# Kernel optimization log

Measured on AMD Instinct MI355X. Metric: run time of the kernel, lower is better.

## Reference

```python
import jax, jax.numpy as jnp
import numpy as np

N_NODES = 100000
N_EDGES = 1600000
IN_DIM = 128
HID = 64
OUT_DIM = 3


def _glorot(key, shape):
    fan_in, fan_out = shape[0], shape[1]
    std = (2.0 / (fan_in + fan_out)) ** 0.5
    return jax.random.normal(key, shape, jnp.float32) * std


def setup_inputs() -> dict:
    key = jax.random.key(0)
    ks = jax.random.split(key, 12)
    x = jax.random.normal(ks[0], (N_NODES, IN_DIM), jnp.float32)
    edge_index = jax.random.randint(ks[1], (2, N_EDGES), 0, N_NODES, dtype=jnp.int32)
    return {
        "x": x,
        "edge_index": edge_index,
        "W1": _glorot(ks[2], (IN_DIM, HID)), "b1": jnp.zeros((HID,), jnp.float32),
        "W2": _glorot(ks[3], (HID, HID)), "b2": jnp.zeros((HID,), jnp.float32),
        "W3": _glorot(ks[4], (HID, HID)), "b3": jnp.zeros((HID,), jnp.float32),
        "W4": _glorot(ks[5], (HID, HID // 2)), "b4": jnp.zeros((HID // 2,), jnp.float32),
        "Wh": _glorot(ks[6], (HID // 2, OUT_DIM)), "bh": jnp.zeros((OUT_DIM,), jnp.float32),
    }


def reference(x, edge_index, W1, b1, W2, b2, W3, b3, W4, b4, Wh, bh):
    n = x.shape[0]
    self_loops = jnp.arange(n, dtype=edge_index.dtype)
    src = jnp.concatenate([edge_index[0], self_loops])  # message sources j
    dst = jnp.concatenate([edge_index[1], self_loops])  # aggregation targets i
    # symmetric GCN normalization with self-loops: deg over targets (unit edge weights)
    deg = jax.ops.segment_sum(jnp.ones_like(dst, jnp.float32), dst, num_segments=n)
    dinv = jnp.where(deg > 0, jax.lax.rsqrt(deg), 0.0)
    norm = dinv[src] * dinv[dst]  # [E+N]

    def gcn(h, W, b):
        h = h @ W  # transform first (PyG GCNConv order)
        agg = jax.ops.segment_sum(h[src] * norm[:, None], dst, num_segments=n)
        return agg + b

    h = jax.nn.relu(gcn(x, W1, b1))   # dropout is identity in eval mode
    h = jax.nn.relu(gcn(h, W2, b2))
    h = jax.nn.relu(gcn(h, W3, b3))
    h = jax.nn.relu(gcn(h, W4, b4))
    return h @ Wh + bh  # [N, 3]
```

## Files before the change

kernel.cpp:

```cpp
#include <hip/hip_runtime.h>
#include <hip/hip_bf16.h>
#include <hip/hip_fp16.h>
#include <cstdint>


#define MAXD 512
#define EB   8192
#define PADSLACK 2048

typedef _Float16 half8v __attribute__((ext_vector_type(8)));
typedef _Float16 half2v __attribute__((ext_vector_type(2)));
typedef float    float4v __attribute__((ext_vector_type(4)));

#if defined(__has_builtin)
#if __has_builtin(__builtin_amdgcn_fdot2)
#define HAVE_FDOT2 1
#endif
#endif

__device__ __forceinline__ float fdot2f(half2v a, half2v b, float c) {
#ifdef HAVE_FDOT2
    return __builtin_amdgcn_fdot2(a, b, c, false);
#else
    return c + (float)a[0] * (float)b[0] + (float)a[1] * (float)b[1];
#endif
}

__device__ __forceinline__ void digit_base_scan(const int* __restrict__ totals,
                                                int ND, int* pairs, int* cbs) {
    const int t = threadIdx.x;
    const int e0 = 2 * t, e1 = 2 * t + 1;
    int v0 = (e0 < ND) ? totals[e0] : 0;
    int v1 = (e1 < ND) ? totals[e1] : 0;
    pairs[t] = v0 + v1;
    __syncthreads();
    for (int off = 1; off < 256; off <<= 1) {
        int x = (t >= off) ? pairs[t - off] : 0;
        __syncthreads();
        pairs[t] += x;
        __syncthreads();
    }
    int ep = pairs[t] - v0 - v1;
    cbs[e0] = ep;
    cbs[e1] = ep + v0;
    __syncthreads();
}

__device__ __forceinline__ void hist_body(const int* __restrict__ ei,
                                          int* __restrict__ histM, int E, int b) {
    __shared__ int hist[MAXD];
    const int tid = threadIdx.x;
    hist[tid] = 0; hist[tid + 256] = 0;
    __syncthreads();
    const int base = b * EB;
#pragma unroll 2
    for (int it = 0; it < EB / 256; it += 4) {
        int d[4]; bool ok[4];
#pragma unroll
        for (int u = 0; u < 4; ++u) {
            int e = base + (it + u) * 256 + tid;
            ok[u] = e < E;
            d[u] = ok[u] ? ei[E + e] : 0;
        }
#pragma unroll
        for (int u = 0; u < 4; ++u)
            if (ok[u]) atomicAdd(&hist[d[u] >> 8], 1);
    }
    __syncthreads();
    histM[(size_t)b * MAXD + tid] = hist[tid];
    histM[(size_t)b * MAXD + tid + 256] = hist[tid + 256];
}

__global__ __launch_bounds__(256) void scan_digits_k(int* __restrict__ histM,
                                                     int* __restrict__ totals,
                                                     int NBLK) {
    __shared__ int s[256];
    const int t = threadIdx.x, dg = blockIdx.x;
    int v = (t < NBLK) ? histM[(size_t)t * MAXD + dg] : 0;
    s[t] = v;
    __syncthreads();
    for (int off = 1; off < 256; off <<= 1) {
        int x = (t >= off) ? s[t - off] : 0;
        __syncthreads();
        s[t] += x;
        __syncthreads();
    }
    if (t < NBLK) histM[(size_t)t * MAXD + dg] = s[t] - v;
    if (t == 255) totals[dg] = s[255];
}

template <int K, int OUT>
__device__ __forceinline__ void gemm_body(const float* __restrict__ H,
                                          const float* __restrict__ W,
                                          float* __restrict__ Tout, int n, int bx) {
    constexpr int TX  = OUT / 4;
    constexpr int TY  = 256 / TX;
    constexpr int BM  = TY * 4;
    constexpr int BK  = 32;
    constexpr int PAD = 4;

    __shared__ float At[BK][BM + PAD];
    __shared__ float Ws[BK][OUT];

    const int t    = threadIdx.x;
    const int cx   = t % TX;
    const int ry   = t / TX;
    const int row0 = bx * BM;

    float acc[4][4] = {{0.f}};
    const int arow = t >> 3;
    const int af4  = t & 7;

    for (int k0 = 0; k0 < K; k0 += BK) {
#pragma unroll
        for (int p = 0; p < BM / 32; ++p) {
            int r  = arow + p * 32;
            int gr = row0 + r;
            int grc = gr < n ? gr : n - 1;
            float4 v = *reinterpret_cast<const float4*>(
                H + (size_t)grc * K + k0 + af4 * 4);
            At[af4 * 4 + 0][r] = v.x;
            At[af4 * 4 + 1][r] = v.y;
            At[af4 * 4 + 2][r] = v.z;
            At[af4 * 4 + 3][r] = v.w;
        }
#pragma unroll
        for (int p = 0; p < (BK * OUT) / 1024; ++p) {
            int idx = t + p * 256;
            int wk  = idx / (OUT / 4);
            int wf  = idx % (OUT / 4);
            float4 v = *reinterpret_cast<const float4*>(
                W + (size_t)(k0 + wk) * OUT + wf * 4);
            *reinterpret_cast<float4*>(&Ws[wk][wf * 4]) = v;
        }
        __syncthreads();
#pragma unroll
        for (int k = 0; k < BK; ++k) {
            float4 a = *reinterpret_cast<const float4*>(&At[k][ry * 4]);
            float4 w = *reinterpret_cast<const float4*>(&Ws[k][cx * 4]);
            acc[0][0] = fmaf(a.x, w.x, acc[0][0]);
            acc[0][1] = fmaf(a.x, w.y, acc[0][1]);
            acc[0][2] = fmaf(a.x, w.z, acc[0][2]);
            acc[0][3] = fmaf(a.x, w.w, acc[0][3]);
            acc[1][0] = fmaf(a.y, w.x, acc[1][0]);
            acc[1][1] = fmaf(a.y, w.y, acc[1][1]);
            acc[1][2] = fmaf(a.y, w.z, acc[1][2]);
            acc[1][3] = fmaf(a.y, w.w, acc[1][3]);
            acc[2][0] = fmaf(a.z, w.x, acc[2][0]);
            acc[2][1] = fmaf(a.z, w.y, acc[2][1]);
            acc[2][2] = fmaf(a.z, w.z, acc[2][2]);
            acc[2][3] = fmaf(a.z, w.w, acc[2][3]);
            acc[3][0] = fmaf(a.w, w.x, acc[3][0]);
            acc[3][1] = fmaf(a.w, w.y, acc[3][1]);
            acc[3][2] = fmaf(a.w, w.z, acc[3][2]);
            acc[3][3] = fmaf(a.w, w.w, acc[3][3]);
        }
        __syncthreads();
    }
#pragma unroll
    for (int i = 0; i < 4; ++i) {
        int gr = row0 + ry * 4 + i;
        if (gr < n) {
            float4 v = make_float4(acc[i][0], acc[i][1], acc[i][2], acc[i][3]);
            *reinterpret_cast<float4*>(Tout + (size_t)gr * OUT + cx * 4) = v;
        }
    }
}

__device__ __forceinline__ void pack_body(const int* __restrict__ ei,
                                          const int* __restrict__ histM,
                                          const int* __restrict__ totals,
                                          int* __restrict__ packed,
                                          int E, int ND, int b) {
    __shared__ int pairs[256];
    __shared__ int cbs[MAXD];
    __shared__ int cur[MAXD];
    const int tid = threadIdx.x;
    digit_base_scan(totals, ND, pairs, cbs);
    for (int t = tid; t < ND; t += 256)
        cur[t] = cbs[t] + histM[(size_t)b * MAXD + t];
    __syncthreads();
    const int base = b * EB;
    for (int it = 0; it < EB / 256; it += 4) {
        int s[4], d[4]; bool ok[4];
#pragma unroll
        for (int u = 0; u < 4; ++u) {
            int e = base + (it + u) * 256 + tid;
            ok[u] = e < E;
            if (ok[u]) { s[u] = ei[e]; d[u] = ei[E + e]; }
        }
#pragma unroll
        for (int u = 0; u < 4; ++u) {
            if (ok[u]) {
                int pos = atomicAdd(&cur[d[u] >> 8], 1);
                packed[pos] = (s[u] << 8) | (d[u] & 255);
            }
        }
    }
}

__global__ __launch_bounds__(256) void hist_gemm1_k(
    const int* __restrict__ ei, int* __restrict__ histM, int E,
    const float* __restrict__ x, const float* __restrict__ W1,
    float* __restrict__ T1, int n, int NH) {
    const int bx = blockIdx.x;
    if (bx < NH) hist_body(ei, histM, E, bx);
    else         gemm_body<128, 64>(x, W1, T1, n, bx - NH);
}

__global__ __launch_bounds__(256) void pack_gemm1_k(
    const int* __restrict__ ei, const int* __restrict__ histM,
    const int* __restrict__ totals, int* __restrict__ packed,
    const float* __restrict__ x, const float* __restrict__ W1,
    float* __restrict__ T1, int n, int E, int ND, int NPB, int G1) {
    const int bx = blockIdx.x;
    if (bx < NPB) pack_body(ei, histM, totals, packed, E, ND, bx);
    else          gemm_body<128, 64>(x, W1, T1, n, G1 + bx - NPB);
}

__global__ __launch_bounds__(256) void bucket_k(const int* __restrict__ packed,
                                                const int* __restrict__ totals,
                                                int ND,
                                                int* __restrict__ col,
                                                int* __restrict__ rowptr,
                                                int* __restrict__ counts,
                                                float* __restrict__ dinv,
                                                const float* __restrict__ Traw,
                                                __half* __restrict__ Th, int n) {
    __shared__ int   pairs[256];
    __shared__ int   cbs[MAXD];
    __shared__ int   hist[256];
    __shared__ int   pref[256];
    __shared__ int   cur[256];
    __shared__ float dinv_l[256];

    const int tid = threadIdx.x;
    const int dg  = blockIdx.x;
    digit_base_scan(totals, ND, pairs, cbs);
    const int base  = cbs[dg];
    const int m     = totals[dg];
    const int basep = base + dg * PADSLACK;

    hist[tid] = 0;
    __syncthreads();
    for (int k0 = 0; k0 < m; k0 += 1024) {
        int v[4]; bool ok[4];
#pragma unroll
        for (int u = 0; u < 4; ++u) {
            int k = k0 + u * 256 + tid;
            ok[u] = k < m;
            v[u] = ok[u] ? packed[base + k] : 0;
        }
#pragma unroll
        for (int u = 0; u < 4; ++u)
            if (ok[u]) atomicAdd(&hist[v[u] & 255], 1);
    }
    __syncthreads();
    const int deg   = hist[tid];
    const int cnt_p = (deg + 8) & ~7;
    pref[tid] = cnt_p;
    __syncthreads();
    for (int off = 1; off < 256; off <<= 1) {
        int x = (tid >= off) ? pref[tid - off] : 0;
        __syncthreads();
        pref[tid] += x;
        __syncthreads();
    }
    const int rp = basep + pref[tid] - cnt_p;
    const float di = rsqrtf((float)(deg + 1));
    dinv_l[tid] = di;
    cur[tid] = rp + 1;
    const int d = dg * 256 + tid;
    if (d < n) {
        counts[d] = cnt_p;
        dinv[d]   = di;
        rowptr[d] = rp;
        col[rp]   = d;
        for (int k = deg + 1; k < cnt_p; ++k) col[rp + k] = n;
    }
    __syncthreads();
    for (int k0 = 0; k0 < m; k0 += 1024) {
        int v[4]; bool ok[4];
#pragma unroll
        for (int u = 0; u < 4; ++u) {
            int k = k0 + u * 256 + tid;
            ok[u] = k < m;
            v[u] = ok[u] ? packed[base + k] : 0;
        }
#pragma unroll
        for (int u = 0; u < 4; ++u) {
            if (ok[u]) {
                int pos = atomicAdd(&cur[v[u] & 255], 1);
                col[pos] = v[u] >> 8;
            }
        }
    }
    const int r0 = dg * 256;
#pragma unroll 4
    for (int it = 0; it < 16; ++it) {
        int idx = it * 256 + tid;
        int rl  = idx >> 4;
        int r   = r0 + rl;
        if (r < n) {
            float4 v = reinterpret_cast<const float4*>(Traw)[(size_t)r * 16 + (idx & 15)];
            float dd = dinv_l[rl];
            union { ushort4 u; __half h[4]; } pk;
            pk.h[0] = __float2half_rn(v.x * dd);
            pk.h[1] = __float2half_rn(v.y * dd);
            pk.h[2] = __float2half_rn(v.z * dd);
            pk.h[3] = __float2half_rn(v.w * dd);
            reinterpret_cast<ushort4*>(Th)[(size_t)r * 16 + (idx & 15)] = pk.u;
        }
    }
    if (dg == 0 && tid < 16) {
        uint2 z; z.x = 0u; z.y = 0u;
        reinterpret_cast<uint2*>(Th)[(size_t)n * 16 + tid] = z;
    }
}

template <int OUT>
__global__ __launch_bounds__(256) void gemm_mfma_k(
    const _Float16* __restrict__ H, const float* __restrict__ W,
    const float* __restrict__ dinv, _Float16* __restrict__ T, int n) {
    constexpr int NT = OUT / 16;
    const int lane = threadIdx.x & 63;
    const int m16  = lane & 15;
    const int quad = lane >> 4;
    const int wid  = (blockIdx.x * blockDim.x + threadIdx.x) >> 6;
    const int nw   = (gridDim.x * blockDim.x) >> 6;

    half8v bfrag[NT][2];
#pragma unroll
    for (int t = 0; t < NT; ++t)
#pragma unroll
        for (int h = 0; h < 2; ++h)
#pragma unroll
            for (int j = 0; j < 8; ++j)
                bfrag[t][h][j] = (_Float16)W[(size_t)(h * 32 + quad * 8 + j) * OUT
                                             + t * 16 + m16];

    const int nblk = (n + 15) >> 4;
    for (int rb = wid; rb < nblk; rb += nw) {
        const int r0 = rb * 16;
        int ra = r0 + m16; if (ra >= n) ra = n - 1;
        const half8v* hrow = reinterpret_cast<const half8v*>(H + (size_t)ra * 64);
        half8v a0 = hrow[quad];
        half8v a1 = hrow[4 + quad];

        float4v dfr[NT];
#pragma unroll
        for (int t = 0; t < NT; ++t) {
            float4v z = {0.f, 0.f, 0.f, 0.f};
            z = __builtin_amdgcn_mfma_f32_16x16x32_f16(a0, bfrag[t][0], z, 0, 0, 0);
            z = __builtin_amdgcn_mfma_f32_16x16x32_f16(a1, bfrag[t][1], z, 0, 0, 0);
            dfr[t] = z;
        }
#pragma unroll
        for (int reg = 0; reg < 4; ++reg) {
            int row = r0 + quad * 4 + reg;
            if (row < n) {
                float di = dinv[row];
#pragma unroll
                for (int t = 0; t < NT; ++t)
                    T[(size_t)row * 64 + t * 16 + m16] =
                        (_Float16)(dfr[t][reg] * di);
            }
        }
    }
}

template <int NB, int LR>
__device__ __forceinline__ void gather_batch(int c_l, const uint2* __restrict__ T2,
                                             int q, int sw, float4& acc) {
    constexpr int NSW = 64 / LR;
    constexpr int GPE = 8 / NSW;
    constexpr int NV  = NB * GPE;
    const half2v s10 = {(_Float16)1.f, (_Float16)0.f};
    const half2v s01 = {(_Float16)0.f, (_Float16)1.f};
    uint2 v[NV];
#pragma unroll
    for (int g = 0; g < NB; ++g)
#pragma unroll
        for (int u = 0; u < GPE; ++u) {
            int cc = __shfl(c_l, g * 8 + u * NSW + sw, 64);
            v[g * GPE + u] = T2[(size_t)cc * 16 + q];
        }
#pragma unroll
    for (int k = 0; k < NV; ++k) {
        union { uint2 uu; half2v h[2]; } cv; cv.uu = v[k];
        acc.x = fdot2f(cv.h[0], s10, acc.x);
        acc.y = fdot2f(cv.h[0], s01, acc.y);
        acc.z = fdot2f(cv.h[1], s10, acc.z);
        acc.w = fdot2f(cv.h[1], s01, acc.w);
    }
}

template <int LR, bool FUSE_HEAD>
__global__ __launch_bounds__(256) void agg_k(const __half* __restrict__ T,
                                             const int* __restrict__ rowptr,
                                             const int* __restrict__ counts,
                                             const int* __restrict__ col,
                                             const float* __restrict__ dinv,
                                             const float* __restrict__ bias,
                                             void* __restrict__ O, int n,
                                             const float* __restrict__ Wh,
                                             const float* __restrict__ bh) {
    constexpr int NSW = 64 / LR;
    constexpr int GPE = 8 / NSW;
    const int lane = threadIdx.x & 63;
    const int q    = lane % LR;
    const int sw   = lane / LR;
    const int i = (blockIdx.x * blockDim.x + threadIdx.x) >> 6;
    if (i >= n) return;

    const int start = rowptr[i];
    const int cnt   = counts[i];
    const uint2* __restrict__ T2 = reinterpret_cast<const uint2*>(T);

    float4 acc = make_float4(0.f, 0.f, 0.f, 0.f);
    if (cnt <= 64) {
        int c_l = col[start + lane];
        switch (cnt >> 3) {
            case 1: gather_batch<1, LR>(c_l, T2, q, sw, acc); break;
            case 2: gather_batch<2, LR>(c_l, T2, q, sw, acc); break;
            case 3: gather_batch<3, LR>(c_l, T2, q, sw, acc); break;
            case 4: gather_batch<4, LR>(c_l, T2, q, sw, acc); break;
            case 5: gather_batch<5, LR>(c_l, T2, q, sw, acc); break;
            case 6: gather_batch<6, LR>(c_l, T2, q, sw, acc); break;
            case 7: gather_batch<7, LR>(c_l, T2, q, sw, acc); break;
            default: gather_batch<8, LR>(c_l, T2, q, sw, acc); break;
        }
    } else {
        const half2v s10 = {(_Float16)1.f, (_Float16)0.f};
        const half2v s01 = {(_Float16)0.f, (_Float16)1.f};
        for (int base = 0; base < cnt; base += 64) {
            const int m = min(64, cnt - base);
            int c_l = col[start + base + lane];
            for (int jg = 0; jg < m; jg += 8) {
                int cc[GPE]; uint2 v[GPE];
#pragma unroll
                for (int u = 0; u < GPE; ++u)
                    cc[u] = __shfl(c_l, jg + u * NSW + sw, 64);
#pragma unroll
                for (int u = 0; u < GPE; ++u) v[u] = T2[(size_t)cc[u] * 16 + q];
#pragma unroll
                for (int u = 0; u < GPE; ++u) {
                    union { uint2 uu; half2v h[2]; } cv; cv.uu = v[u];
                    acc.x = fdot2f(cv.h[0], s10, acc.x);
                    acc.y = fdot2f(cv.h[0], s01, acc.y);
                    acc.z = fdot2f(cv.h[1], s10, acc.z);
                    acc.w = fdot2f(cv.h[1], s01, acc.w);
                }
            }
        }
    }
#pragma unroll
    for (int off = LR; off < 64; off <<= 1) {
        acc.x += __shfl_xor(acc.x, off, 64);
        acc.y += __shfl_xor(acc.y, off, 64);
        acc.z += __shfl_xor(acc.z, off, 64);
        acc.w += __shfl_xor(acc.w, off, 64);
    }
    const float di = dinv[i];
    const float4 b4 = reinterpret_cast<const float4*>(bias)[q];
    float4 h;
    h.x = fmaxf(fmaf(di, acc.x, b4.x), 0.f);
    h.y = fmaxf(fmaf(di, acc.y, b4.y), 0.f);
    h.z = fmaxf(fmaf(di, acc.z, b4.z), 0.f);
    h.w = fmaxf(fmaf(di, acc.w, b4.w), 0.f);
    if constexpr (!FUSE_HEAD) {
        if (sw == 0) {
            union { ushort4 u; __half hh[4]; } pk;
            pk.hh[0] = __float2half_rn(h.x);
            pk.hh[1] = __float2half_rn(h.y);
            pk.hh[2] = __float2half_rn(h.z);
            pk.hh[3] = __float2half_rn(h.w);
            ushort* base_p = (ushort*)O + (size_t)i * 64;
            *reinterpret_cast<ushort4*>(base_p + 4 * q) = pk.u;
        }
    } else {
        float* Of = (float*)O;
        float p0 = h.x * Wh[(4 * q + 0) * 3 + 0];
        float p1 = h.x * Wh[(4 * q + 0) * 3 + 1];
        float p2 = h.x * Wh[(4 * q + 0) * 3 + 2];
        p0 = fmaf(h.y, Wh[(4 * q + 1) * 3 + 0], p0);
        p1 = fmaf(h.y, Wh[(4 * q + 1) * 3 + 1], p1);
        p2 = fmaf(h.y, Wh[(4 * q + 1) * 3 + 2], p2);
        p0 = fmaf(h.z, Wh[(4 * q + 2) * 3 + 0], p0);
        p1 = fmaf(h.z, Wh[(4 * q + 2) * 3 + 1], p1);
        p2 = fmaf(h.z, Wh[(4 * q + 2) * 3 + 2], p2);
        p0 = fmaf(h.w, Wh[(4 * q + 3) * 3 + 0], p0);
        p1 = fmaf(h.w, Wh[(4 * q + 3) * 3 + 1], p1);
        p2 = fmaf(h.w, Wh[(4 * q + 3) * 3 + 2], p2);
#pragma unroll
        for (int off = 1; off < LR; off <<= 1) {
            p0 += __shfl_xor(p0, off, 64);
            p1 += __shfl_xor(p1, off, 64);
            p2 += __shfl_xor(p2, off, 64);
        }
        if (lane == 0) {
            Of[(size_t)i * 3 + 0] = p0 + bh[0];
            Of[(size_t)i * 3 + 1] = p1 + bh[1];
            Of[(size_t)i * 3 + 2] = p2 + bh[2];
        }
    }
}

extern "C" void kernel_launch(void* const* d_in, const int* in_sizes, int n_in,
                              void* d_out, int out_size, void* d_ws, size_t ws_size,
                              hipStream_t stream) {
    const float* x  = (const float*)d_in[0];
    const int*   ei = (const int*)d_in[1];
    const float* W1 = (const float*)d_in[2];
    const float* b1 = (const float*)d_in[3];
    const float* W2 = (const float*)d_in[4];
    const float* b2 = (const float*)d_in[5];
    const float* W3 = (const float*)d_in[6];
    const float* b3 = (const float*)d_in[7];
    const float* W4 = (const float*)d_in[8];
    const float* b4 = (const float*)d_in[9];
    const float* Wh = (const float*)d_in[10];
    const float* bh = (const float*)d_in[11];
    float* out = (float*)d_out;

    const int n = in_sizes[0] / 128;
    const int E = in_sizes[1] / 2;
    const int ND   = (n + 255) / 256;
    const int NBLK = (E + EB - 1) / EB;

    char* ws = (char*)d_ws;
    auto alloc = [&](size_t bytes) {
        char* p = ws;
        ws += (bytes + 255) & ~(size_t)255;
        return p;
    };
    int*    histM  = (int*)alloc((size_t)NBLK * MAXD * 4);
    int*    totals = (int*)alloc((size_t)MAXD * 4);
    int*    packed = (int*)alloc((size_t)E * 4);
    int*    col    = (int*)alloc(((size_t)E + (size_t)ND * PADSLACK + 256) * 4);
    int*    rowptr = (int*)alloc((size_t)n * 4);
    int*    counts = (int*)alloc((size_t)n * 4);
    float*  dinv   = (float*)alloc((size_t)n * 4);
    float*  bufF   = (float*)alloc((size_t)n * 64 * 4);
    __half* bufH   = (__half*)alloc(((size_t)n + 1) * 64 * 2);
    __half* bufG   = (__half*)bufF;

    dim3 blk(256);
    const int G  = (n + 63) / 64;
    const int G1 = G / 3;
    const int G2 = G - G1;
    const int agg_blocks = (n + 3) / 4;
    const int mfma_blocks = 640;

    hist_gemm1_k<<<dim3(NBLK + G1), blk, 0, stream>>>(ei, histM, E, x, W1, bufF, n, NBLK);
    scan_digits_k<<<dim3(ND), blk, 0, stream>>>(histM, totals, NBLK);
    pack_gemm1_k<<<dim3(NBLK + G2), blk, 0, stream>>>(ei, histM, totals, packed,
                                                      x, W1, bufF, n, E, ND, NBLK, G1);
    bucket_k<<<dim3(ND), blk, 0, stream>>>(packed, totals, ND, col, rowptr, counts,
                                           dinv, bufF, bufH, n);
    agg_k<16, false><<<dim3(agg_blocks), blk, 0, stream>>>(
        bufH, rowptr, counts, col, dinv, b1, bufG, n, nullptr, nullptr);
    gemm_mfma_k<64><<<dim3(mfma_blocks), blk, 0, stream>>>(
        (const _Float16*)bufG, W2, dinv, (_Float16*)bufH, n);
    agg_k<16, false><<<dim3(agg_blocks), blk, 0, stream>>>(
        bufH, rowptr, counts, col, dinv, b2, bufG, n, nullptr, nullptr);
    gemm_mfma_k<64><<<dim3(mfma_blocks), blk, 0, stream>>>(
        (const _Float16*)bufG, W3, dinv, (_Float16*)bufH, n);
    agg_k<16, false><<<dim3(agg_blocks), blk, 0, stream>>>(
        bufH, rowptr, counts, col, dinv, b3, bufG, n, nullptr, nullptr);
    gemm_mfma_k<32><<<dim3(mfma_blocks), blk, 0, stream>>>(
        (const _Float16*)bufG, W4, dinv, (_Float16*)bufH, n);
    agg_k<8, true><<<dim3(agg_blocks), blk, 0, stream>>>(
        bufH, rowptr, counts, col, dinv, b4, out, n, Wh, bh);
}
```

Before: 349.2 us.

## Make aggregation persistent with prefetched row metadata and packed row descriptors

The aggregation kernel now runs as a grid-stride persistent loop over 2048 blocks. Each wave prefetches the next rows' packed (rowptr, count, dinv) int4 descriptor and column indices, so those dependent loads overlap the current row's gather. The bucket kernel writes this packed descriptor in place of the separate rowptr, counts and dinv reads. Gather batches are capped at 4 groups to reduce register pressure, with a launch bound of 8 waves per SIMD. A leftover unused helper, gather_node, is also added.

```diff
diff --git a/kernel.cpp b/kernel.cpp
--- a/kernel.cpp
+++ b/kernel.cpp
@@ -222,8 +222,7 @@
                                                 const int* __restrict__ totals,
                                                 int ND,
                                                 int* __restrict__ col,
-                                                int* __restrict__ rowptr,
-                                                int* __restrict__ counts,
+                                                int4* __restrict__ rpc,
                                                 float* __restrict__ dinv,
                                                 const float* __restrict__ Traw,
                                                 __half* __restrict__ Th, int n) {
@@ -272,10 +271,9 @@
     cur[tid] = rp + 1;
     const int d = dg * 256 + tid;
     if (d < n) {
-        counts[d] = cnt_p;
-        dinv[d]   = di;
-        rowptr[d] = rp;
-        col[rp]   = d;
+        rpc[d]  = make_int4(rp, cnt_p, __float_as_int(di), 0);
+        dinv[d] = di;
+        col[rp] = d;
         for (int k = deg + 1; k < cnt_p; ++k) col[rp + k] = n;
     }
     __syncthreads();
@@ -371,7 +369,7 @@
 
 template <int NB, int LR>
 __device__ __forceinline__ void gather_batch(int c_l, const uint2* __restrict__ T2,
-                                             int q, int sw, float4& acc) {
+                                             int q, int sw, float4& acc, int g0) {
     constexpr int NSW = 64 / LR;
     constexpr int GPE = 8 / NSW;
     constexpr int NV  = NB * GPE;
@@ -382,7 +380,7 @@
     for (int g = 0; g < NB; ++g)
 #pragma unroll
         for (int u = 0; u < GPE; ++u) {
-            int cc = __shfl(c_l, g * 8 + u * NSW + sw, 64);
+            int cc = __shfl(c_l, (g0 + g) * 8 + u * NSW + sw, 64);
             v[g * GPE + u] = T2[(size_t)cc * 16 + q];
         }
 #pragma unroll
@@ -395,12 +393,22 @@
     }
 }
 
+__device__ __forceinline__ void gather_node(int cnt, int start, int c_a,
+                                            const uint2* __restrict__ T2,
+                                            const int* __restrict__ col,
+                                            int lane, int q, int sw, float4& acc) {
+    if (cnt <= 64) {
+        switch (cnt >> 3) {
+            case 1: gather_batch<1, 64 / ((64/16))>(c_a, T2, q, sw, acc, 0); break;
+            default: break;
+        }
+    }
+}
+
 template <int LR, bool FUSE_HEAD>
-__global__ __launch_bounds__(256) void agg_k(const __half* __restrict__ T,
-                                             const int* __restrict__ rowptr,
-                                             const int* __restrict__ counts,
+__global__ __launch_bounds__(256, 8) void agg_k(const __half* __restrict__ T,
+                                             const int4* __restrict__ rpc,
                                              const int* __restrict__ col,
-                                             const float* __restrict__ dinv,
                                              const float* __restrict__ bias,
                                              void* __restrict__ O, int n,
                                              const float* __restrict__ Wh,
@@ -410,99 +418,108 @@
     const int lane = threadIdx.x & 63;
     const int q    = lane % LR;
     const int sw   = lane / LR;
-    const int i = (blockIdx.x * blockDim.x + threadIdx.x) >> 6;
-    if (i >= n) return;
-
-    const int start = rowptr[i];
-    const int cnt   = counts[i];
+    const int wid  = (blockIdx.x * blockDim.x + threadIdx.x) >> 6;
+    const int nw   = (gridDim.x * blockDim.x) >> 6;
+    if (wid >= n) return;
+
     const uint2* __restrict__ T2 = reinterpret_cast<const uint2*>(T);
-
-    float4 acc = make_float4(0.f, 0.f, 0.f, 0.f);
-    if (cnt <= 64) {
-        int c_l = col[start + lane];
-        switch (cnt >> 3) {
-            case 1: gather_batch<1, LR>(c_l, T2, q, sw, acc); break;
-            case 2: gather_batch<2, LR>(c_l, T2, q, sw, acc); break;
-            case 3: gather_batch<3, LR>(c_l, T2, q, sw, acc); break;
-            case 4: gather_batch<4, LR>(c_l, T2, q, sw, acc); break;
-            case 5: gather_batch<5, LR>(c_l, T2, q, sw, acc); break;
-            case 6: gather_batch<6, LR>(c_l, T2, q, sw, acc); break;
-            case 7: gather_batch<7, LR>(c_l, T2, q, sw, acc); break;
-            default: gather_batch<8, LR>(c_l, T2, q, sw, acc); break;
-        }
-    } else {
-        const half2v s10 = {(_Float16)1.f, (_Float16)0.f};
-        const half2v s01 = {(_Float16)0.f, (_Float16)1.f};
-        for (int base = 0; base < cnt; base += 64) {
-            const int m = min(64, cnt - base);
-            int c_l = col[start + base + lane];
-            for (int jg = 0; jg < m; jg += 8) {
-                int cc[GPE]; uint2 v[GPE];
-#pragma unroll
-                for (int u = 0; u < GPE; ++u)
-                    cc[u] = __shfl(c_l, jg + u * NSW + sw, 64);
-#pragma unroll
-                for (int u = 0; u < GPE; ++u) v[u] = T2[(size_t)cc[u] * 16 + q];
-#pragma unroll
-                for (int u = 0; u < GPE; ++u) {
-                    union { uint2 uu; half2v h[2]; } cv; cv.uu = v[u];
-                    acc.x = fdot2f(cv.h[0], s10, acc.x);
-                    acc.y = fdot2f(cv.h[0], s01, acc.y);
-                    acc.z = fdot2f(cv.h[1], s10, acc.z);
-                    acc.w = fdot2f(cv.h[1], s01, acc.w);
+    const float4 b4 = reinterpret_cast<const float4*>(bias)[q];
+
+    int ib = wid + nw; if (ib >= n) ib = n - 1;
+    int4 rc_a = rpc[wid];
+    int4 rc_b = rpc[ib];
+    int  c_a  = col[rc_a.x + lane];
+
+    for (int i = wid; i < n; i += nw) {
+        int ic = i + 2 * nw; if (ic >= n) ic = n - 1;
+        int4 rc_c = rpc[ic];
+        int  c_nx = col[rc_b.x + lane];
+
+        const int   cnt   = rc_a.y;
+        const int   start = rc_a.x;
+        const float di    = __int_as_float(rc_a.z);
+
+        float4 acc = make_float4(0.f, 0.f, 0.f, 0.f);
+        if (cnt <= 64) {
+            switch (cnt >> 3) {
+                case 1: gather_batch<1, LR>(c_a, T2, q, sw, acc, 0); break;
+                case 2: gather_batch<2, LR>(c_a, T2, q, sw, acc, 0); break;
+                case 3: gather_batch<3, LR>(c_a, T2, q, sw, acc, 0); break;
+                case 4: gather_batch<4, LR>(c_a, T2, q, sw, acc, 0); break;
+                case 5: gather_batch<4, LR>(c_a, T2, q, sw, acc, 0);
+                        gather_batch<1, LR>(c_a, T2, q, sw, acc, 4); break;
+                case 6: gather_batch<4, LR>(c_a, T2, q, sw, acc, 0);
+                        gather_batch<2, LR>(c_a, T2, q, sw, acc, 4); break;
+                case 7: gather_batch<4, LR>(c_a, T2, q, sw, acc, 0);
+                        gather_batch<3, LR>(c_a, T2, q, sw, acc, 4); break;
+                default: gather_batch<4, LR>(c_a, T2, q, sw, acc, 0);
+                         gather_batch<4, LR>(c_a, T2, q, sw, acc, 4); break;
+            }
+        } else {
+            for (int base = 0; base < cnt; base += 64) {
+                int m = cnt - base; if (m > 64) m = 64;
+                int c_l = col[start + base + lane];
+                for (int jg = 0; jg < m; jg += 32) {
+                    int nb2 = (m - jg) >> 3; if (nb2 > 4) nb2 = 4;
+                    int g0 = jg >> 3;
+                    switch (nb2) {
+                        case 1: gather_batch<1, LR>(c_l, T2, q, sw, acc, g0); break;
+                        case 2: gather_batch<2, LR>(c_l, T2, q, sw, acc, g0); break;
+                        case 3: gather_batch<3, LR>(c_l, T2, q, sw, acc, g0); break;
+                        default: gather_batch<4, LR>(c_l, T2, q, sw, acc, g0); break;
+                    }
                 }
             }
         }
-    }
-#pragma unroll
-    for (int off = LR; off < 64; off <<= 1) {
-        acc.x += __shfl_xor(acc.x, off, 64);
-        acc.y += __shfl_xor(acc.y, off, 64);
-        acc.z += __shfl_xor(acc.z, off, 64);
-        acc.w += __shfl_xor(acc.w, off, 64);
-    }
-    const float di = dinv[i];
-    const float4 b4 = reinterpret_cast<const float4*>(bias)[q];
-    float4 h;
-    h.x = fmaxf(fmaf(di, acc.x, b4.x), 0.f);
-    h.y = fmaxf(fmaf(di, acc.y, b4.y), 0.f);
-    h.z = fmaxf(fmaf(di, acc.z, b4.z), 0.f);
-    h.w = fmaxf(fmaf(di, acc.w, b4.w), 0.f);
-    if constexpr (!FUSE_HEAD) {
-        if (sw == 0) {
-            union { ushort4 u; __half hh[4]; } pk;
-            pk.hh[0] = __float2half_rn(h.x);
-            pk.hh[1] = __float2half_rn(h.y);
-            pk.hh[2] = __float2half_rn(h.z);
-            pk.hh[3] = __float2half_rn(h.w);
-            ushort* base_p = (ushort*)O + (size_t)i * 64;
-            *reinterpret_cast<ushort4*>(base_p + 4 * q) = pk.u;
-        }
-    } else {
-        float* Of = (float*)O;
-        float p0 = h.x * Wh[(4 * q + 0) * 3 + 0];
-        float p1 = h.x * Wh[(4 * q + 0) * 3 + 1];
-        float p2 = h.x * Wh[(4 * q + 0) * 3 + 2];
-        p0 = fmaf(h.y, Wh[(4 * q + 1) * 3 + 0], p0);
-        p1 = fmaf(h.y, Wh[(4 * q + 1) * 3 + 1], p1);
-        p2 = fmaf(h.y, Wh[(4 * q + 1) * 3 + 2], p2);
-        p0 = fmaf(h.z, Wh[(4 * q + 2) * 3 + 0], p0);
-        p1 = fmaf(h.z, Wh[(4 * q + 2) * 3 + 1], p1);
-        p2 = fmaf(h.z, Wh[(4 * q + 2) * 3 + 2], p2);
-        p0 = fmaf(h.w, Wh[(4 * q + 3) * 3 + 0], p0);
-        p1 = fmaf(h.w, Wh[(4 * q + 3) * 3 + 1], p1);
-        p2 = fmaf(h.w, Wh[(4 * q + 3) * 3 + 2], p2);
-#pragma unroll
-        for (int off = 1; off < LR; off <<= 1) {
-            p0 += __shfl_xor(p0, off, 64);
-            p1 += __shfl_xor(p1, off, 64);
-            p2 += __shfl_xor(p2, off, 64);
-        }
-        if (lane == 0) {
-            Of[(size_t)i * 3 + 0] = p0 + bh[0];
-            Of[(size_t)i * 3 + 1] = p1 + bh[1];
-            Of[(size_t)i * 3 + 2] = p2 + bh[2];
-        }
+#pragma unroll
+        for (int off = LR; off < 64; off <<= 1) {
+            acc.x += __shfl_xor(acc.x, off, 64);
+            acc.y += __shfl_xor(acc.y, off, 64);
+            acc.z += __shfl_xor(acc.z, off, 64);
+            acc.w += __shfl_xor(acc.w, off, 64);
+        }
+        float4 h;
+        h.x = fmaxf(fmaf(di, acc.x, b4.x), 0.f);
+        h.y = fmaxf(fmaf(di, acc.y, b4.y), 0.f);
+        h.z = fmaxf(fmaf(di, acc.z, b4.z), 0.f);
+        h.w = fmaxf(fmaf(di, acc.w, b4.w), 0.f);
+        if constexpr (!FUSE_HEAD) {
+            if (sw == 0) {
+                union { ushort4 u; __half hh[4]; } pk;
+                pk.hh[0] = __float2half_rn(h.x);
+                pk.hh[1] = __float2half_rn(h.y);
+                pk.hh[2] = __float2half_rn(h.z);
+                pk.hh[3] = __float2half_rn(h.w);
+                ushort* base_p = (ushort*)O + (size_t)i * 64;
+                *reinterpret_cast<ushort4*>(base_p + 4 * q) = pk.u;
+            }
+        } else {
+            float* Of = (float*)O;
+            float p0 = h.x * Wh[(4 * q + 0) * 3 + 0];
+            float p1 = h.x * Wh[(4 * q + 0) * 3 + 1];
+            float p2 = h.x * Wh[(4 * q + 0) * 3 + 2];
+            p0 = fmaf(h.y, Wh[(4 * q + 1) * 3 + 0], p0);
+            p1 = fmaf(h.y, Wh[(4 * q + 1) * 3 + 1], p1);
+            p2 = fmaf(h.y, Wh[(4 * q + 1) * 3 + 2], p2);
+            p0 = fmaf(h.z, Wh[(4 * q + 2) * 3 + 0], p0);
+            p1 = fmaf(h.z, Wh[(4 * q + 2) * 3 + 1], p1);
+            p2 = fmaf(h.z, Wh[(4 * q + 2) * 3 + 2], p2);
+            p0 = fmaf(h.w, Wh[(4 * q + 3) * 3 + 0], p0);
+            p1 = fmaf(h.w, Wh[(4 * q + 3) * 3 + 1], p1);
+            p2 = fmaf(h.w, Wh[(4 * q + 3) * 3 + 2], p2);
+#pragma unroll
+            for (int off = 1; off < LR; off <<= 1) {
+                p0 += __shfl_xor(p0, off, 64);
+                p1 += __shfl_xor(p1, off, 64);
+                p2 += __shfl_xor(p2, off, 64);
+            }
+            if (lane == 0) {
+                Of[(size_t)i * 3 + 0] = p0 + bh[0];
+                Of[(size_t)i * 3 + 1] = p1 + bh[1];
+                Of[(size_t)i * 3 + 2] = p2 + bh[2];
+            }
+        }
+        rc_a = rc_b; rc_b = rc_c; c_a = c_nx;
     }
 }
 
@@ -538,8 +555,7 @@
     int*    totals = (int*)alloc((size_t)MAXD * 4);
     int*    packed = (int*)alloc((size_t)E * 4);
     int*    col    = (int*)alloc(((size_t)E + (size_t)ND * PADSLACK + 256) * 4);
-    int*    rowptr = (int*)alloc((size_t)n * 4);
-    int*    counts = (int*)alloc((size_t)n * 4);
+    int4*   rpc    = (int4*)alloc((size_t)n * 16);
     float*  dinv   = (float*)alloc((size_t)n * 4);
     float*  bufF   = (float*)alloc((size_t)n * 64 * 4);
     __half* bufH   = (__half*)alloc(((size_t)n + 1) * 64 * 2);
@@ -549,27 +565,27 @@
     const int G  = (n + 63) / 64;
     const int G1 = G / 3;
     const int G2 = G - G1;
-    const int agg_blocks = (n + 3) / 4;
+    const int agg_blocks = 2048;
     const int mfma_blocks = 640;
 
     hist_gemm1_k<<<dim3(NBLK + G1), blk, 0, stream>>>(ei, histM, E, x, W1, bufF, n, NBLK);
     scan_digits_k<<<dim3(ND), blk, 0, stream>>>(histM, totals, NBLK);
     pack_gemm1_k<<<dim3(NBLK + G2), blk, 0, stream>>>(ei, histM, totals, packed,
                                                       x, W1, bufF, n, E, ND, NBLK, G1);
-    bucket_k<<<dim3(ND), blk, 0, stream>>>(packed, totals, ND, col, rowptr, counts,
+    bucket_k<<<dim3(ND), blk, 0, stream>>>(packed, totals, ND, col, rpc,
                                            dinv, bufF, bufH, n);
     agg_k<16, false><<<dim3(agg_blocks), blk, 0, stream>>>(
-        bufH, rowptr, counts, col, dinv, b1, bufG, n, nullptr, nullptr);
+        bufH, rpc, col, b1, bufG, n, nullptr, nullptr);
     gemm_mfma_k<64><<<dim3(mfma_blocks), blk, 0, stream>>>(
         (const _Float16*)bufG, W2, dinv, (_Float16*)bufH, n);
     agg_k<16, false><<<dim3(agg_blocks), blk, 0, stream>>>(
-        bufH, rowptr, counts, col, dinv, b2, bufG, n, nullptr, nullptr);
+        bufH, rpc, col, b2, bufG, n, nullptr, nullptr);
     gemm_mfma_k<64><<<dim3(mfma_blocks), blk, 0, stream>>>(
         (const _Float16*)bufG, W3, dinv, (_Float16*)bufH, n);
     agg_k<16, false><<<dim3(agg_blocks), blk, 0, stream>>>(
-        bufH, rowptr, counts, col, dinv, b3, bufG, n, nullptr, nullptr);
+        bufH, rpc, col, b3, bufG, n, nullptr, nullptr);
     gemm_mfma_k<32><<<dim3(mfma_blocks), blk, 0, stream>>>(
         (const _Float16*)bufG, W4, dinv, (_Float16*)bufH, n);
     agg_k<8, true><<<dim3(agg_blocks), blk, 0, stream>>>(
-        bufH, rowptr, counts, col, dinv, b4, out, n, Wh, bh);
-}
+        bufH, rpc, col, b4, out, n, Wh, bh);
+}
```

After: 334.5 us. 4.2% less time.
